# Kernel optimization log

Measured on AMD Instinct MI355X. Metric: run time of the kernel, lower is better.

The kernel has to match this reference:

```python
import jax, jax.numpy as jnp
import numpy as np

B, C, CI, H, W = 4, 128, 64, 64, 64


def conv1x1(x, w, b):
    # x: [B,C,H,W], w: [Cout,Cin], b: [Cout]
    return jnp.einsum('bchw,oc->bohw', x, w) + b[None, :, None, None]


def setup_inputs() -> dict:
    key = jax.random.key(0)
    ks = jax.random.split(key, 10)
    s = 0.05  # keep logits in a sane range for softmax
    return {
        'x0': jax.random.normal(ks[0], (B, C, H, W), jnp.float32),
        'x1': jax.random.normal(ks[1], (B, C, H, W), jnp.float32),
        'g_w': jax.random.normal(ks[2], (CI, C), jnp.float32) * s,
        'g_b': jax.random.normal(ks[3], (CI,), jnp.float32) * s,
        'theta_w': jax.random.normal(ks[4], (CI, C), jnp.float32) * s,
        'theta_b': jax.random.normal(ks[5], (CI,), jnp.float32) * s,
        'phi_w': jax.random.normal(ks[6], (CI, C), jnp.float32) * s,
        'phi_b': jax.random.normal(ks[7], (CI,), jnp.float32) * s,
        'W_w': jax.random.normal(ks[8], (C, CI), jnp.float32) * s,
        'W_b': jax.random.normal(ks[9], (C,), jnp.float32) * s,
    }


def reference(x0, x1, g_w, g_b, theta_w, theta_b, phi_w, phi_b, W_w, W_b):
    b, c, h, w = x0.shape
    n = h * w
    ci = g_w.shape[0]
    g_x = conv1x1(x0, g_w, g_b).reshape(b, ci, n).transpose(0, 2, 1)      # [B,N,Ci]
    theta_x = conv1x1(x1, theta_w, theta_b).reshape(b, ci, n).transpose(0, 2, 1)  # [B,N,Ci]
    phi_x = conv1x1(x0, phi_w, phi_b).reshape(b, ci, n)                    # [B,Ci,N]
    f = jnp.einsum('bqc,bck->bqk', theta_x, phi_x)                         # [B,N,N]
    f_div_C = jax.nn.softmax(f, axis=-1)
    y = jnp.einsum('bqk,bkc->bqc', f_div_C, g_x)                           # [B,N,Ci]
    y = y.transpose(0, 2, 1).reshape(b, ci, h, w)
    W_y = conv1x1(y, W_w, W_b)
    return W_y + x0
```

## Files before the change

### kernel.cpp

```cpp
#include <hip/hip_runtime.h>
#include <hip/hip_bf16.h>


typedef unsigned int   u32;
typedef unsigned short u16;
typedef __attribute__((ext_vector_type(8))) short short8;
typedef __attribute__((ext_vector_type(4))) short short4v;
typedef __attribute__((ext_vector_type(4))) float f32x4;

#define LOG2E 1.4426950408889634f
#define KSPLIT 8

__device__ __forceinline__ float b2f(u16 v) {
  union { u32 u; float f; } x; x.u = ((u32)v) << 16; return x.f;
}
__device__ __forceinline__ u16 f2b(float f) {
  u32 u = __float_as_uint(f);
  return (u16)((u + 0x8000u) >> 16);
}
__device__ __forceinline__ short8 load_w_frag(const float* p, float s) {
  const float4 f0 = ((const float4*)p)[0];
  const float4 f1 = ((const float4*)p)[1];
  union { u32 w[4]; short8 s8; } r;
  r.w[0] = (u32)f2b(f0.x * s) | ((u32)f2b(f0.y * s) << 16);
  r.w[1] = (u32)f2b(f0.z * s) | ((u32)f2b(f0.w * s) << 16);
  r.w[2] = (u32)f2b(f1.x * s) | ((u32)f2b(f1.y * s) << 16);
  r.w[3] = (u32)f2b(f1.z * s) | ((u32)f2b(f1.w * s) << 16);
  return r.s8;
}


__global__ __launch_bounds__(256) void qkv_fused_kernel(
    const float* __restrict__ x0, const float* __restrict__ x1,
    const float* __restrict__ tw, const float* __restrict__ tb,
    const float* __restrict__ pw, const float* __restrict__ pb,
    const float* __restrict__ gw, const float* __restrict__ gb,
    u16* __restrict__ Q, u16* __restrict__ K, u16* __restrict__ Vt)
{
  const int n0 = blockIdx.x * 64;
  const int b  = blockIdx.y;
  const int t  = threadIdx.x;

  __shared__ __align__(16) short xt[2][64][136];

  #pragma unroll
  for (int i = 0; i < 16; ++i) {
    const int idx = i * 256 + t;
    const int tensor = idx >> 11;
    const int c  = (idx >> 4) & 127;
    const int n4 = idx & 15;
    const float4 v = *(const float4*)(
        (tensor ? x1 : x0) + ((size_t)b * 128 + c) * 4096 + n0 + n4 * 4);
    short* d = &xt[tensor][n4 * 4][c];
    d[0]       = (short)f2b(v.x);
    d[136]     = (short)f2b(v.y);
    d[2 * 136] = (short)f2b(v.z);
    d[3 * 136] = (short)f2b(v.w);
  }
  asm volatile("" ::: "memory");
  __syncthreads();

  const int wave = t >> 6;
  const int lane = t & 63;
  const int quad = lane >> 4, l15 = lane & 15;

  if (wave < 2) {
    const int conv = wave;
    const float* wsrc = conv ? pw : tw;
    const float  ws   = conv ? 1.f : LOG2E;
    const short* xl   = &xt[conv ? 0 : 1][0][0];

    f32x4 acc[4][4];
    #pragma unroll
    for (int i = 0; i < 4; ++i)
      #pragma unroll
      for (int j = 0; j < 4; ++j) acc[i][j] = (f32x4){0.f, 0.f, 0.f, 0.f};

    #pragma unroll
    for (int kk = 0; kk < 4; ++kk) {
      short8 wf[4], xf[4];
      #pragma unroll
      for (int ot = 0; ot < 4; ++ot)
        wf[ot] = load_w_frag(wsrc + (ot * 16 + l15) * 128 + kk * 32 + quad * 8, ws);
      #pragma unroll
      for (int nt = 0; nt < 4; ++nt)
        xf[nt] = *(const short8*)(xl + (nt * 16 + l15) * 136 + kk * 32 + quad * 8);
      #pragma unroll
      for (int i = 0; i < 4; ++i)
        #pragma unroll
        for (int j = 0; j < 4; ++j)
          acc[i][j] = __builtin_amdgcn_mfma_f32_16x16x32_bf16(xf[i], wf[j], acc[i][j], 0, 0, 0);
    }

    u16* dst = (conv ? K : Q) + (size_t)b * 4096 * 64;
    const float* bias = conv ? pb : tb;
    const float bscale = conv ? 1.f : LOG2E;
    #pragma unroll
    for (int ot = 0; ot < 4; ++ot) {
      const float bv = bias[ot * 16 + l15] * bscale;
      #pragma unroll
      for (int nt = 0; nt < 4; ++nt)
        #pragma unroll
        for (int r = 0; r < 4; ++r) {
          const int n = n0 + nt * 16 + quad * 4 + r;
          dst[(size_t)n * 64 + ot * 16 + l15] = f2b(acc[nt][ot][r] + bv);
        }
    }
  } else {
    const int oh = wave - 2;
    const short* xl = &xt[0][0][0];

    f32x4 acc[2][4];
    #pragma unroll
    for (int i = 0; i < 2; ++i)
      #pragma unroll
      for (int j = 0; j < 4; ++j) acc[i][j] = (f32x4){0.f, 0.f, 0.f, 0.f};

    #pragma unroll
    for (int kk = 0; kk < 4; ++kk) {
      short8 wf[2], xf[4];
      #pragma unroll
      for (int ot = 0; ot < 2; ++ot)
        wf[ot] = load_w_frag(gw + ((oh * 2 + ot) * 16 + l15) * 128 + kk * 32 + quad * 8, 1.f);
      #pragma unroll
      for (int nt = 0; nt < 4; ++nt)
        xf[nt] = *(const short8*)(xl + (nt * 16 + l15) * 136 + kk * 32 + quad * 8);
      #pragma unroll
      for (int i = 0; i < 2; ++i)
        #pragma unroll
        for (int j = 0; j < 4; ++j)
          acc[i][j] = __builtin_amdgcn_mfma_f32_16x16x32_bf16(wf[i], xf[j], acc[i][j], 0, 0, 0);
    }

    u16* dst = Vt + (size_t)b * 64 * 4096;
    #pragma unroll
    for (int ot = 0; ot < 2; ++ot)
      #pragma unroll
      for (int r = 0; r < 4; ++r) {
        const int o = (oh * 2 + ot) * 16 + quad * 4 + r;
        const float bv = gb[o];
        #pragma unroll
        for (int nc = 0; nc < 4; ++nc)
          dst[(size_t)o * 4096 + n0 + nc * 16 + l15] = f2b(acc[ot][nc][r] + bv);
      }
  }
}

__global__ __launch_bounds__(256) void attn_kernel(
    const u16* __restrict__ Q, const u16* __restrict__ K,
    const u16* __restrict__ Vt, u16* __restrict__ Opart,
    float* __restrict__ Lp)
{
  const int qt = blockIdx.x, b = blockIdx.y, ks = blockIdx.z;
  const int tid  = threadIdx.x;
  const int wave = tid >> 6;
  const int lane = tid & 63;
  const int quad = lane >> 4;
  const int l15  = lane & 15;

  __shared__ __align__(16) short K_lds[2][64][72];
  __shared__ __align__(16) short V_lds[2][64][72];
  __shared__ __align__(16) short P_lds[4][64][72];
  short* pw = &P_lds[wave][0][0];

  const int q0 = qt * 256 + wave * 64;
  const u16* Qb = Q  + (size_t)b * 4096 * 64;
  const u16* Kb = K  + (size_t)b * 4096 * 64;
  const u16* Vb = Vt + (size_t)b * 64 * 4096;

  const int kbase = ks * (4096 / KSPLIT);
  const int NKT   = 4096 / KSPLIT / 64;

  const int r0 = tid >> 3;
  const int c0 = tid & 7;

  short8 qf[4][2];
  #pragma unroll
  for (int nt = 0; nt < 4; ++nt) {
    const u16* qp = Qb + (size_t)(q0 + nt * 16 + l15) * 64 + quad * 8;
    qf[nt][0] = *(const short8*)qp;
    qf[nt][1] = *(const short8*)(qp + 32);
  }

  f32x4 oacc[4][4];
  #pragma unroll
  for (int i = 0; i < 4; ++i)
    #pragma unroll
    for (int j = 0; j < 4; ++j)
      oacc[i][j] = (f32x4){0.f, 0.f, 0.f, 0.f};
  float lsum[4] = {0.f, 0.f, 0.f, 0.f};

  {
    const u16* kg = Kb + (size_t)kbase * 64;
    uint4 ka0 = *(const uint4*)(kg + (size_t)r0 * 64 + c0 * 8);
    uint4 ka1 = *(const uint4*)(kg + (size_t)(r0 + 32) * 64 + c0 * 8);
    uint4 va0 = *(const uint4*)(Vb + (size_t)r0 * 4096 + kbase + c0 * 8);
    uint4 va1 = *(const uint4*)(Vb + (size_t)(r0 + 32) * 4096 + kbase + c0 * 8);
    *(uint4*)&K_lds[0][r0][c0 * 8]      = ka0;
    *(uint4*)&K_lds[0][r0 + 32][c0 * 8] = ka1;
    *(uint4*)&V_lds[0][r0][c0 * 8]      = va0;
    *(uint4*)&V_lds[0][r0 + 32][c0 * 8] = va1;
  }
  __syncthreads();

  for (int kt = 0; kt < NKT; ++kt) {
    const int buf = kt & 1;
    const bool pre = (kt + 1 < NKT);

    uint4 ka0, ka1, va0, va1;
    if (pre) {
      const int k1 = kbase + (kt + 1) * 64;
      const u16* kg = Kb + (size_t)k1 * 64;
      ka0 = *(const uint4*)(kg + (size_t)r0 * 64 + c0 * 8);
      ka1 = *(const uint4*)(kg + (size_t)(r0 + 32) * 64 + c0 * 8);
      va0 = *(const uint4*)(Vb + (size_t)r0 * 4096 + k1 + c0 * 8);
      va1 = *(const uint4*)(Vb + (size_t)(r0 + 32) * 4096 + k1 + c0 * 8);
    }

    short8 kf[4][2];
    #pragma unroll
    for (int mt = 0; mt < 4; ++mt) {
      kf[mt][0] = *(const short8*)&K_lds[buf][mt * 16 + l15][quad * 8];
      kf[mt][1] = *(const short8*)&K_lds[buf][mt * 16 + l15][quad * 8 + 32];
    }

    #pragma unroll
    for (int mt = 0; mt < 4; ++mt) {
      #pragma unroll
      for (int nt = 0; nt < 4; ++nt) {
        f32x4 s = {0.f, 0.f, 0.f, 0.f};
        s = __builtin_amdgcn_mfma_f32_16x16x32_bf16(kf[mt][0], qf[nt][0], s, 0, 0, 0);
        s = __builtin_amdgcn_mfma_f32_16x16x32_bf16(kf[mt][1], qf[nt][1], s, 0, 0, 0);
        float p0 = exp2f(s[0]), p1 = exp2f(s[1]), p2 = exp2f(s[2]), p3 = exp2f(s[3]);
        lsum[nt] += (p0 + p1) + (p2 + p3);
        u32 u0 = __float_as_uint(p0) + 0x8000u;
        u32 u1 = __float_as_uint(p1) + 0x8000u;
        u32 u2 = __float_as_uint(p2) + 0x8000u;
        u32 u3 = __float_as_uint(p3) + 0x8000u;
        union { uint2 u; short4v s4; } pk;
        pk.u.x = __builtin_amdgcn_perm(u1, u0, 0x07060302u);
        pk.u.y = __builtin_amdgcn_perm(u3, u2, 0x07060302u);
        *(short4v*)(pw + (nt * 16 + l15) * 72 + mt * 16 + quad * 4) = pk.s4;
      }
    }

    asm volatile("" ::: "memory");

    short8 vf[4][2];
    #pragma unroll
    for (int nd = 0; nd < 4; ++nd) {
      vf[nd][0] = *(const short8*)&V_lds[buf][nd * 16 + l15][quad * 8];
      vf[nd][1] = *(const short8*)&V_lds[buf][nd * 16 + l15][quad * 8 + 32];
    }

    #pragma unroll
    for (int mq = 0; mq < 4; ++mq) {
      const short* pr = pw + (mq * 16 + l15) * 72 + quad * 8;
      short8 pa0 = *(const short8*)pr;
      short8 pa1 = *(const short8*)(pr + 32);
      #pragma unroll
      for (int nd = 0; nd < 4; ++nd) {
        oacc[mq][nd] = __builtin_amdgcn_mfma_f32_16x16x32_bf16(pa0, vf[nd][0], oacc[mq][nd], 0, 0, 0);
        oacc[mq][nd] = __builtin_amdgcn_mfma_f32_16x16x32_bf16(pa1, vf[nd][1], oacc[mq][nd], 0, 0, 0);
      }
    }

    asm volatile("" ::: "memory");

    __syncthreads();
    if (pre) {
      const int nb = buf ^ 1;
      *(uint4*)&K_lds[nb][r0][c0 * 8]      = ka0;
      *(uint4*)&K_lds[nb][r0 + 32][c0 * 8] = ka1;
      *(uint4*)&V_lds[nb][r0][c0 * 8]      = va0;
      *(uint4*)&V_lds[nb][r0 + 32][c0 * 8] = va1;
      __syncthreads();
    }
  }

  #pragma unroll
  for (int nt = 0; nt < 4; ++nt) {
    float v = lsum[nt];
    v += __shfl_xor(v, 16, 64);
    v += __shfl_xor(v, 32, 64);
    lsum[nt] = v;
  }
  float* LpB = Lp + ((size_t)ks * 4 + b) * 4096;
  if (quad == 0) {
    #pragma unroll
    for (int nt = 0; nt < 4; ++nt)
      LpB[q0 + nt * 16 + l15] = lsum[nt];
  }

  u16* Ob = Opart + ((size_t)ks * 4 + b) * 4096 * 64;
  #pragma unroll
  for (int mq = 0; mq < 4; ++mq)
    #pragma unroll
    for (int nd = 0; nd < 4; ++nd)
      #pragma unroll
      for (int r = 0; r < 4; ++r) {
        int q = q0 + mq * 16 + quad * 4 + r;
        Ob[(size_t)q * 64 + nd * 16 + l15] = f2b(oacc[mq][nd][r]);
      }
}

__global__ __launch_bounds__(256) void out_fused_kernel(
    const u16* __restrict__ Opart, const float* __restrict__ Lp,
    const float* __restrict__ Wf, const float* __restrict__ Wbf,
    const float* __restrict__ x0, float* __restrict__ out)
{
  const int n0 = blockIdx.x * 64;
  const int b  = blockIdx.y;
  const int t  = threadIdx.x;

  __shared__ __align__(16) short Ys[64][72];

  {
    const int nl = t >> 2;
    const int q4 = t & 3;
    const int ng = n0 + nl;

    float l = 0.f;
    #pragma unroll
    for (int ks = 0; ks < KSPLIT; ++ks)
      l += Lp[((size_t)ks * 4 + b) * 4096 + ng];

    float a[16];
    #pragma unroll
    for (int j = 0; j < 16; ++j) a[j] = 0.f;
    #pragma unroll
    for (int ks = 0; ks < KSPLIT; ++ks) {
      const uint4* row = (const uint4*)(Opart + (((size_t)ks * 4 + b) * 4096 + ng) * 64 + q4 * 16);
      #pragma unroll
      for (int v = 0; v < 2; ++v) {
        uint4 r = row[v];
        u32 wds[4] = {r.x, r.y, r.z, r.w};
        #pragma unroll
        for (int j = 0; j < 4; ++j) {
          a[v * 8 + 2 * j]     += __uint_as_float(wds[j] << 16);
          a[v * 8 + 2 * j + 1] += __uint_as_float(wds[j] & 0xffff0000u);
        }
      }
    }
    const float rinv = 1.f / l;
    union { u32 w[8]; short8 s8[2]; } pk;
    #pragma unroll
    for (int j = 0; j < 8; ++j)
      pk.w[j] = (u32)f2b(a[2 * j] * rinv) | ((u32)f2b(a[2 * j + 1] * rinv) << 16);
    *(short8*)&Ys[nl][q4 * 16]     = pk.s8[0];
    *(short8*)&Ys[nl][q4 * 16 + 8] = pk.s8[1];
  }
  asm volatile("" ::: "memory");
  __syncthreads();

  const int wave = t >> 6;
  const int lane = t & 63;
  const int quad = lane >> 4, l15 = lane & 15;

  f32x4 acc[2][4];
  #pragma unroll
  for (int i = 0; i < 2; ++i)
    #pragma unroll
    for (int j = 0; j < 4; ++j) acc[i][j] = (f32x4){0.f, 0.f, 0.f, 0.f};

  #pragma unroll
  for (int kk = 0; kk < 2; ++kk) {
    short8 wf[2], yf[4];
    #pragma unroll
    for (int ot = 0; ot < 2; ++ot)
      wf[ot] = load_w_frag(Wf + ((wave * 2 + ot) * 16 + l15) * 64 + kk * 32 + quad * 8, 1.f);
    #pragma unroll
    for (int nt = 0; nt < 4; ++nt)
      yf[nt] = *(const short8*)&Ys[nt * 16 + l15][kk * 32 + quad * 8];
    #pragma unroll
    for (int i = 0; i < 2; ++i)
      #pragma unroll
      for (int j = 0; j < 4; ++j)
        acc[i][j] = __builtin_amdgcn_mfma_f32_16x16x32_bf16(wf[i], yf[j], acc[i][j], 0, 0, 0);
  }

  #pragma unroll
  for (int ot = 0; ot < 2; ++ot)
    #pragma unroll
    for (int r = 0; r < 4; ++r) {
      const int o = (wave * 2 + ot) * 16 + quad * 4 + r;
      const float bv = Wbf[o];
      #pragma unroll
      for (int nt = 0; nt < 4; ++nt) {
        const size_t idx = ((size_t)(b * 128 + o)) * 4096 + n0 + nt * 16 + l15;
        out[idx] = acc[ot][nt][r] + bv + x0[idx];
      }
    }
}

extern "C" void kernel_launch(void* const* d_in, const int* in_sizes, int n_in,
                              void* d_out, int out_size, void* d_ws, size_t ws_size,
                              hipStream_t stream) {
  const float* x0 = (const float*)d_in[0];
  const float* x1 = (const float*)d_in[1];
  const float* gw = (const float*)d_in[2];
  const float* gb = (const float*)d_in[3];
  const float* tw = (const float*)d_in[4];
  const float* tb = (const float*)d_in[5];
  const float* pw = (const float*)d_in[6];
  const float* pb = (const float*)d_in[7];
  const float* Ww = (const float*)d_in[8];
  const float* Wb = (const float*)d_in[9];
  float* out = (float*)d_out;

  char* ws = (char*)d_ws;
  u16*   Qw    = (u16*)(ws + 0);
  u16*   Kw    = (u16*)(ws + (2u << 20));
  u16*   Vtw   = (u16*)(ws + (4u << 20));
  u16*   Opart = (u16*)(ws + (6u << 20));
  float* Lp    = (float*)(ws + (22u << 20));

  qkv_fused_kernel<<<dim3(64, 4), dim3(256), 0, stream>>>(
      x0, x1, tw, tb, pw, pb, gw, gb, Qw, Kw, Vtw);

  attn_kernel<<<dim3(16, 4, KSPLIT), dim3(256), 0, stream>>>(Qw, Kw, Vtw, Opart, Lp);

  out_fused_kernel<<<dim3(64, 4), dim3(256), 0, stream>>>(
      Opart, Lp, Ww, Wb, x0, out);
}
```

Measured before the change: 133.5 us.

## Shrink attention tile to 32 queries per wave and single-buffer K/V LDS

The attention kernel now gives each wave 32 queries instead of 64, which doubles the grid along the query axis. K/V LDS drops from double to single buffering, and P staging shrinks by processing keys in two 32-key halves. launch_bounds(256,4) asks for four blocks per CU. The aim is to cut registers and LDS so occupancy and block count rise. In exchange each K/V tile loaded into LDS is reused by half as many queries, so K/V global traffic doubles.

```diff
diff --git a/kernel.cpp b/kernel.cpp
--- a/kernel.cpp
+++ b/kernel.cpp
@@ -146,7 +146,7 @@
   }
 }
 
-__global__ __launch_bounds__(256) void attn_kernel(
+__global__ __launch_bounds__(256, 4) void attn_kernel(
     const u16* __restrict__ Q, const u16* __restrict__ K,
     const u16* __restrict__ Vt, u16* __restrict__ Opart,
     float* __restrict__ Lp)
@@ -158,12 +158,12 @@
   const int quad = lane >> 4;
   const int l15  = lane & 15;
 
-  __shared__ __align__(16) short K_lds[2][64][72];
-  __shared__ __align__(16) short V_lds[2][64][72];
-  __shared__ __align__(16) short P_lds[4][64][72];
+  __shared__ __align__(16) short K_lds[64][72];
+  __shared__ __align__(16) short V_lds[64][72];
+  __shared__ __align__(16) short P_lds[4][32][40];
   short* pw = &P_lds[wave][0][0];
 
-  const int q0 = qt * 256 + wave * 64;
+  const int q0 = qt * 128 + wave * 32;
   const u16* Qb = Q  + (size_t)b * 4096 * 64;
   const u16* Kb = K  + (size_t)b * 4096 * 64;
   const u16* Vb = Vt + (size_t)b * 64 * 4096;
@@ -171,115 +171,108 @@
   const int kbase = ks * (4096 / KSPLIT);
   const int NKT   = 4096 / KSPLIT / 64;
 
-  const int r0 = tid >> 3;
-  const int c0 = tid & 7;
-
-  short8 qf[4][2];
-  #pragma unroll
-  for (int nt = 0; nt < 4; ++nt) {
+  const int sr = tid >> 2;
+  const int sc = (tid & 3) * 8;
+
+  short8 qf[2][2];
+  #pragma unroll
+  for (int nt = 0; nt < 2; ++nt) {
     const u16* qp = Qb + (size_t)(q0 + nt * 16 + l15) * 64 + quad * 8;
     qf[nt][0] = *(const short8*)qp;
     qf[nt][1] = *(const short8*)(qp + 32);
   }
 
-  f32x4 oacc[4][4];
-  #pragma unroll
-  for (int i = 0; i < 4; ++i)
+  f32x4 oacc[2][4];
+  #pragma unroll
+  for (int i = 0; i < 2; ++i)
     #pragma unroll
     for (int j = 0; j < 4; ++j)
       oacc[i][j] = (f32x4){0.f, 0.f, 0.f, 0.f};
-  float lsum[4] = {0.f, 0.f, 0.f, 0.f};
+  float lsum[2] = {0.f, 0.f};
 
   {
     const u16* kg = Kb + (size_t)kbase * 64;
-    uint4 ka0 = *(const uint4*)(kg + (size_t)r0 * 64 + c0 * 8);
-    uint4 ka1 = *(const uint4*)(kg + (size_t)(r0 + 32) * 64 + c0 * 8);
-    uint4 va0 = *(const uint4*)(Vb + (size_t)r0 * 4096 + kbase + c0 * 8);
-    uint4 va1 = *(const uint4*)(Vb + (size_t)(r0 + 32) * 4096 + kbase + c0 * 8);
-    *(uint4*)&K_lds[0][r0][c0 * 8]      = ka0;
-    *(uint4*)&K_lds[0][r0 + 32][c0 * 8] = ka1;
-    *(uint4*)&V_lds[0][r0][c0 * 8]      = va0;
-    *(uint4*)&V_lds[0][r0 + 32][c0 * 8] = va1;
+    uint4 ka = *(const uint4*)(kg + (size_t)sr * 64 + sc);
+    uint4 kb = *(const uint4*)(kg + (size_t)sr * 64 + sc + 32);
+    uint4 va = *(const uint4*)(Vb + (size_t)sr * 4096 + kbase + sc);
+    uint4 vb = *(const uint4*)(Vb + (size_t)sr * 4096 + kbase + sc + 32);
+    *(uint4*)&K_lds[sr][sc]      = ka;
+    *(uint4*)&K_lds[sr][sc + 32] = kb;
+    *(uint4*)&V_lds[sr][sc]      = va;
+    *(uint4*)&V_lds[sr][sc + 32] = vb;
   }
   __syncthreads();
 
   for (int kt = 0; kt < NKT; ++kt) {
-    const int buf = kt & 1;
     const bool pre = (kt + 1 < NKT);
 
-    uint4 ka0, ka1, va0, va1;
+    uint4 ka, kb, va, vb;
     if (pre) {
       const int k1 = kbase + (kt + 1) * 64;
       const u16* kg = Kb + (size_t)k1 * 64;
-      ka0 = *(const uint4*)(kg + (size_t)r0 * 64 + c0 * 8);
-      ka1 = *(const uint4*)(kg + (size_t)(r0 + 32) * 64 + c0 * 8);
-      va0 = *(const uint4*)(Vb + (size_t)r0 * 4096 + k1 + c0 * 8);
-      va1 = *(const uint4*)(Vb + (size_t)(r0 + 32) * 4096 + k1 + c0 * 8);
-    }
-
-    short8 kf[4][2];
-    #pragma unroll
-    for (int mt = 0; mt < 4; ++mt) {
-      kf[mt][0] = *(const short8*)&K_lds[buf][mt * 16 + l15][quad * 8];
-      kf[mt][1] = *(const short8*)&K_lds[buf][mt * 16 + l15][quad * 8 + 32];
-    }
-
-    #pragma unroll
-    for (int mt = 0; mt < 4; ++mt) {
-      #pragma unroll
-      for (int nt = 0; nt < 4; ++nt) {
-        f32x4 s = {0.f, 0.f, 0.f, 0.f};
-        s = __builtin_amdgcn_mfma_f32_16x16x32_bf16(kf[mt][0], qf[nt][0], s, 0, 0, 0);
-        s = __builtin_amdgcn_mfma_f32_16x16x32_bf16(kf[mt][1], qf[nt][1], s, 0, 0, 0);
-        float p0 = exp2f(s[0]), p1 = exp2f(s[1]), p2 = exp2f(s[2]), p3 = exp2f(s[3]);
-        lsum[nt] += (p0 + p1) + (p2 + p3);
-        u32 u0 = __float_as_uint(p0) + 0x8000u;
-        u32 u1 = __float_as_uint(p1) + 0x8000u;
-        u32 u2 = __float_as_uint(p2) + 0x8000u;
-        u32 u3 = __float_as_uint(p3) + 0x8000u;
-        union { uint2 u; short4v s4; } pk;
-        pk.u.x = __builtin_amdgcn_perm(u1, u0, 0x07060302u);
-        pk.u.y = __builtin_amdgcn_perm(u3, u2, 0x07060302u);
-        *(short4v*)(pw + (nt * 16 + l15) * 72 + mt * 16 + quad * 4) = pk.s4;
-      }
-    }
-
-    asm volatile("" ::: "memory");
-
-    short8 vf[4][2];
-    #pragma unroll
-    for (int nd = 0; nd < 4; ++nd) {
-      vf[nd][0] = *(const short8*)&V_lds[buf][nd * 16 + l15][quad * 8];
-      vf[nd][1] = *(const short8*)&V_lds[buf][nd * 16 + l15][quad * 8 + 32];
-    }
-
-    #pragma unroll
-    for (int mq = 0; mq < 4; ++mq) {
-      const short* pr = pw + (mq * 16 + l15) * 72 + quad * 8;
-      short8 pa0 = *(const short8*)pr;
-      short8 pa1 = *(const short8*)(pr + 32);
-      #pragma unroll
-      for (int nd = 0; nd < 4; ++nd) {
-        oacc[mq][nd] = __builtin_amdgcn_mfma_f32_16x16x32_bf16(pa0, vf[nd][0], oacc[mq][nd], 0, 0, 0);
-        oacc[mq][nd] = __builtin_amdgcn_mfma_f32_16x16x32_bf16(pa1, vf[nd][1], oacc[mq][nd], 0, 0, 0);
-      }
-    }
-
-    asm volatile("" ::: "memory");
+      ka = *(const uint4*)(kg + (size_t)sr * 64 + sc);
+      kb = *(const uint4*)(kg + (size_t)sr * 64 + sc + 32);
+      va = *(const uint4*)(Vb + (size_t)sr * 4096 + k1 + sc);
+      vb = *(const uint4*)(Vb + (size_t)sr * 4096 + k1 + sc + 32);
+    }
+
+    #pragma unroll
+    for (int kh = 0; kh < 2; ++kh) {
+      short8 kf[2][2], vf[4];
+      #pragma unroll
+      for (int m = 0; m < 2; ++m) {
+        kf[m][0] = *(const short8*)&K_lds[(kh * 2 + m) * 16 + l15][quad * 8];
+        kf[m][1] = *(const short8*)&K_lds[(kh * 2 + m) * 16 + l15][quad * 8 + 32];
+      }
+      #pragma unroll
+      for (int nd = 0; nd < 4; ++nd)
+        vf[nd] = *(const short8*)&V_lds[nd * 16 + l15][kh * 32 + quad * 8];
+
+      #pragma unroll
+      for (int m = 0; m < 2; ++m) {
+        #pragma unroll
+        for (int nt = 0; nt < 2; ++nt) {
+          f32x4 s = {0.f, 0.f, 0.f, 0.f};
+          s = __builtin_amdgcn_mfma_f32_16x16x32_bf16(kf[m][0], qf[nt][0], s, 0, 0, 0);
+          s = __builtin_amdgcn_mfma_f32_16x16x32_bf16(kf[m][1], qf[nt][1], s, 0, 0, 0);
+          float p0 = exp2f(s[0]), p1 = exp2f(s[1]), p2 = exp2f(s[2]), p3 = exp2f(s[3]);
+          lsum[nt] += (p0 + p1) + (p2 + p3);
+          u32 u0 = __float_as_uint(p0) + 0x8000u;
+          u32 u1 = __float_as_uint(p1) + 0x8000u;
+          u32 u2 = __float_as_uint(p2) + 0x8000u;
+          u32 u3 = __float_as_uint(p3) + 0x8000u;
+          union { uint2 u; short4v s4; } pk;
+          pk.u.x = __builtin_amdgcn_perm(u1, u0, 0x07060302u);
+          pk.u.y = __builtin_amdgcn_perm(u3, u2, 0x07060302u);
+          *(short4v*)(pw + (nt * 16 + l15) * 40 + m * 16 + quad * 4) = pk.s4;
+        }
+      }
+
+      asm volatile("" ::: "memory");
+
+      #pragma unroll
+      for (int mq = 0; mq < 2; ++mq) {
+        const short8 pa = *(const short8*)(pw + (mq * 16 + l15) * 40 + quad * 8);
+        #pragma unroll
+        for (int nd = 0; nd < 4; ++nd)
+          oacc[mq][nd] = __builtin_amdgcn_mfma_f32_16x16x32_bf16(pa, vf[nd], oacc[mq][nd], 0, 0, 0);
+      }
+
+      asm volatile("" ::: "memory");
+    }
 
     __syncthreads();
     if (pre) {
-      const int nb = buf ^ 1;
-      *(uint4*)&K_lds[nb][r0][c0 * 8]      = ka0;
-      *(uint4*)&K_lds[nb][r0 + 32][c0 * 8] = ka1;
-      *(uint4*)&V_lds[nb][r0][c0 * 8]      = va0;
-      *(uint4*)&V_lds[nb][r0 + 32][c0 * 8] = va1;
+      *(uint4*)&K_lds[sr][sc]      = ka;
+      *(uint4*)&K_lds[sr][sc + 32] = kb;
+      *(uint4*)&V_lds[sr][sc]      = va;
+      *(uint4*)&V_lds[sr][sc + 32] = vb;
       __syncthreads();
     }
   }
 
   #pragma unroll
-  for (int nt = 0; nt < 4; ++nt) {
+  for (int nt = 0; nt < 2; ++nt) {
     float v = lsum[nt];
     v += __shfl_xor(v, 16, 64);
     v += __shfl_xor(v, 32, 64);
@@ -288,13 +281,13 @@
   float* LpB = Lp + ((size_t)ks * 4 + b) * 4096;
   if (quad == 0) {
     #pragma unroll
-    for (int nt = 0; nt < 4; ++nt)
+    for (int nt = 0; nt < 2; ++nt)
       LpB[q0 + nt * 16 + l15] = lsum[nt];
   }
 
   u16* Ob = Opart + ((size_t)ks * 4 + b) * 4096 * 64;
   #pragma unroll
-  for (int mq = 0; mq < 4; ++mq)
+  for (int mq = 0; mq < 2; ++mq)
     #pragma unroll
     for (int nd = 0; nd < 4; ++nd)
       #pragma unroll
@@ -418,7 +411,7 @@
   qkv_fused_kernel<<<dim3(64, 4), dim3(256), 0, stream>>>(
       x0, x1, tw, tb, pw, pb, gw, gb, Qw, Kw, Vtw);
 
-  attn_kernel<<<dim3(16, 4, KSPLIT), dim3(256), 0, stream>>>(Qw, Kw, Vtw, Opart, Lp);
+  attn_kernel<<<dim3(32, 4, KSPLIT), dim3(256), 0, stream>>>(Qw, Kw, Vtw, Opart, Lp);
 
   out_fused_kernel<<<dim3(64, 4), dim3(256), 0, stream>>>(
       Opart, Lp, Ww, Wb, x0, out);
```

Measured after the change: 128.4 us (median of 2 runs). 1.04x faster.
